# Kernel tuning notes

Measured on AMD Instinct MI355X. Metric: run time of the kernel, lower is better.

The kernel has to match this reference:

```python
import jax, jax.numpy as jnp
import numpy as np

N, E, T, F = 20000, 320000, 64, 16
HG, HT = 128, 256


def setup_inputs() -> dict:
    key = jax.random.key(0)
    ks = jax.random.split(key, 18)
    s = 0.05
    p = lambda k, shape: jax.random.normal(k, shape, jnp.float32) * s
    return {
        "x_seq": jax.random.normal(ks[0], (1, T, N, F), jnp.float32),
        "edge_index": jax.random.randint(ks[1], (2, E), 0, N, jnp.int32),
        # SAGEConv 1 (PyG default: mean aggregation; lin_l on aggregated neighbors w/ bias, lin_r on root w/o bias)
        "W1l": p(ks[2], (HG, F)), "b1l": p(ks[3], (HG,)), "W1r": p(ks[4], (HG, F)),
        # SAGEConv 2
        "W2l": p(ks[5], (HG, HG)), "b2l": p(ks[6], (HG,)), "W2r": p(ks[7], (HG, HG)),
        # GRU (torch gate order: r, z, n)
        "W_ih": p(ks[8], (3 * HT, HG)), "W_hh": p(ks[9], (3 * HT, HT)),
        "b_ih": p(ks[10], (3 * HT,)), "b_hh": p(ks[11], (3 * HT,)),
        # head: Linear(HT,64) -> ReLU -> Linear(64,1)
        "Wh1": p(ks[12], (64, HT)), "bh1": p(ks[13], (64,)),
        "Wh2": p(ks[14], (1, 64)), "bh2": p(ks[15], (1,)),
    }


def reference(x_seq, edge_index, W1l, b1l, W1r, W2l, b2l, W2r,
              W_ih, W_hh, b_ih, b_hh, Wh1, bh1, Wh2, bh2):
    n_nodes = x_seq.shape[2]
    src, dst = edge_index[0], edge_index[1]
    # in-degree for mean aggregation (0 -> output 0, matching scatter-mean)
    deg = jax.ops.segment_sum(jnp.ones(src.shape[0], x_seq.dtype), dst,
                              num_segments=n_nodes)
    inv_deg = jnp.where(deg > 0, 1.0 / deg, 0.0)[:, None]  # [N,1]

    def sage(x, Wl, bl, Wr):
        # mean over incoming neighbor messages, then linear + root linear
        agg = jax.ops.segment_sum(x[src], dst, num_segments=n_nodes) * inv_deg
        return agg @ Wl.T + bl + x @ Wr.T

    def graph_step(carry, x_t):  # x_t: [N, F]
        h = jax.nn.relu(sage(x_t, W1l, b1l, W1r))
        h = jax.nn.relu(sage(h, W2l, b2l, W2r))
        return carry, h.mean(axis=0)  # [HG]

    _, Hg = jax.lax.scan(graph_step, 0, x_seq[0])  # [T, HG]

    hidden_t = W_hh.shape[1]

    def gru_step(h, x_t):
        gi = x_t @ W_ih.T + b_ih
        gh = h @ W_hh.T + b_hh
        i_r, i_z, i_n = jnp.split(gi, 3)
        h_r, h_z, h_n = jnp.split(gh, 3)
        r = jax.nn.sigmoid(i_r + h_r)
        z = jax.nn.sigmoid(i_z + h_z)
        n = jnp.tanh(i_n + r * h_n)
        h_new = (1.0 - z) * n + z * h
        return h_new, h_new

    h0 = jnp.zeros((hidden_t,), x_seq.dtype)
    h_last, _ = jax.lax.scan(gru_step, h0, Hg)  # [HT]

    y = jax.nn.relu(h_last @ Wh1.T + bh1) @ Wh2.T + bh2  # [1]
    return y
```

## Files before the change

kernel.cpp:

```cpp
#include <hip/hip_runtime.h>
#include <hip/hip_bf16.h>

#define N_NODES 20000
#define N_EDGES 320000
#define T_STEPS 64
#define F_IN    16
#define HGd     128
#define HTd     256
#define INVN    (1.0f/20000.0f)
#define NTILES   625
#define S1T      79
#define NG64     313
#define QSCALE   64.0f
#define INVQ     (1.0f/64.0f)
#define QX       32.0f
#define INVQX    (1.0f/32.0f)
#define S_Q8     ((size_t)(N_NODES + 1) * HGd)

typedef __attribute__((ext_vector_type(8))) short short8;
typedef __attribute__((ext_vector_type(4))) float f32x4;
typedef __attribute__((ext_vector_type(2))) float f32x2;
typedef __attribute__((ext_vector_type(2))) _Float16 half2t;

static __device__ __forceinline__ ushort f2bf(float f) {
    __hip_bfloat16 b = __float2bfloat16(f);
    return *reinterpret_cast<ushort*>(&b);
}
static __device__ __forceinline__ half2t u2h(uint u) {
    half2t h; __builtin_memcpy(&h, &u, 4); return h;
}
static __device__ __forceinline__ uint packf16(float a, float b) {
    auto h = __builtin_amdgcn_cvt_pkrtz(a, b);
    uint u; __builtin_memcpy(&u, &h, 4); return u;
}

__global__ void k_zero(int* __restrict__ deg, float* __restrict__ HgP,
                       int* __restrict__ jobc, int* __restrict__ bins,
                       uint* __restrict__ h1q, int tch) {
    int i = blockIdx.x * blockDim.x + threadIdx.x;
    if (i < N_NODES) deg[i] = 0;
    if (i < T_STEPS * 8 * HGd) HgP[i] = 0.0f;
    if (i < 1024) jobc[i] = 0;
    if (i < 256) bins[i] = 0;
    if (i < tch * 32) {
        int sl = i >> 5, j = i & 31;
        h1q[sl * (S_Q8 / 4) + (size_t)N_NODES * (HGd / 4) + j] = 0u;
    }
}

__global__ void k_degree(const int* __restrict__ ei, int* __restrict__ deg) {
    int e = blockIdx.x * blockDim.x + threadIdx.x;
    if (e < N_EDGES) atomicAdd(&deg[ei[N_EDGES + e]], 1);
}

__global__ __launch_bounds__(1024) void k_scan(const int* __restrict__ deg,
        int* __restrict__ rp, int* __restrict__ cursor, float* __restrict__ invd) {
    __shared__ int sh[1024];
    __shared__ int carry_s;
    int tid = threadIdx.x;
    if (tid == 0) { carry_s = 0; rp[0] = 0; }
    __syncthreads();
    for (int base = 0; base < N_NODES; base += 1024) {
        int i = base + tid;
        int v = (i < N_NODES) ? deg[i] : 0;
        sh[tid] = v;
        __syncthreads();
        for (int off = 1; off < 1024; off <<= 1) {
            int t = (tid >= off) ? sh[tid - off] : 0;
            __syncthreads();
            sh[tid] += t;
            __syncthreads();
        }
        int inc = sh[tid] + carry_s;
        if (i < N_NODES) {
            rp[i + 1] = inc;
            cursor[i] = inc - v;
            invd[i] = (v > 0) ? (1.0f / (float)v) : 0.0f;
        }
        __syncthreads();
        if (tid == 1023) carry_s = inc;
        __syncthreads();
    }
}

__global__ void k_fill(const int* __restrict__ ei, int* __restrict__ cursor,
                       int* __restrict__ csr) {
    int e = blockIdx.x * blockDim.x + threadIdx.x;
    if (e < N_EDGES) {
        int d = ei[N_EDGES + e];
        int p = atomicAdd(&cursor[d], 1);
        csr[p] = ei[e];
    }
}

__global__ void k_hist(const int* __restrict__ deg, int* __restrict__ bins) {
    int i = blockIdx.x * blockDim.x + threadIdx.x;
    if (i < N_NODES) atomicAdd(&bins[min(deg[i], 255)], 1);
}

__global__ __launch_bounds__(256) void k_binscan(const int* __restrict__ bins,
        int* __restrict__ bincur, int* __restrict__ nodebefore,
        int* __restrict__ edgebefore, int* __restrict__ edgebp, int* __restrict__ rp2p) {
    __shared__ int sh[256], she[256], shp[256];
    int tid = threadIdx.x;
    int b = bins[tid];
    int dp = (tid + 7) & ~7;
    sh[tid] = b;
    she[tid] = b * tid;
    shp[tid] = b * dp;
    __syncthreads();
    for (int off = 1; off < 256; off <<= 1) {
        int v = (tid >= off) ? sh[tid - off] : 0;
        int ve = (tid >= off) ? she[tid - off] : 0;
        int vp = (tid >= off) ? shp[tid - off] : 0;
        __syncthreads();
        sh[tid] += v; she[tid] += ve; shp[tid] += vp;
        __syncthreads();
    }
    bincur[tid] = sh[tid] - b;
    nodebefore[tid] = sh[tid] - b;
    edgebefore[tid] = she[tid] - b * tid;
    edgebp[tid] = shp[tid] - b * dp;
    if (tid == 255) rp2p[N_NODES] = shp[255];
}

__global__ void k_perm(const int* __restrict__ deg, int* __restrict__ bincur,
                       const int* __restrict__ nodebefore, const int* __restrict__ edgebefore,
                       const int* __restrict__ edgebp, const float* __restrict__ invd,
                       int* __restrict__ perm, int* __restrict__ pos,
                       int* __restrict__ rp2, float* __restrict__ invd2,
                       int* __restrict__ degs2, int* __restrict__ rp2p) {
    int i = blockIdx.x * blockDim.x + threadIdx.x;
    if (i < N_NODES) {
        int d = min(deg[i], 255);
        int p = atomicAdd(&bincur[d], 1);
        int rank = p - nodebefore[d];
        perm[p] = i;
        pos[i] = p;
        rp2[p] = edgebefore[d] + rank * d;
        rp2p[p] = edgebp[d] + rank * ((d + 7) & ~7);
        invd2[p] = invd[i];
        degs2[p] = deg[i];
        if (i == 0) rp2[N_NODES] = N_EDGES;
    }
}

__global__ __launch_bounds__(512) void k_tb(const int* __restrict__ rp2, int* __restrict__ tb) {
    __shared__ int sh[512];
    int t = threadIdx.x;
    int md = 0;
    if (t < NG64 && t * 64 < N_NODES) {
        int last = min((t + 1) * 64, N_NODES) - 1;
        md = rp2[last + 1] - rp2[last];
    }
    sh[t] = 64 * md;
    __syncthreads();
    for (int off = 1; off < 512; off <<= 1) {
        int v = (t >= off) ? sh[t - off] : 0;
        __syncthreads();
        sh[t] += v;
        __syncthreads();
    }
    tb[t + 1] = sh[t];
    if (t == 0) tb[0] = 0;
}

__global__ void k_ecopy(const int* __restrict__ rp, const int* __restrict__ pos,
                        const int* __restrict__ rp2p, const int* __restrict__ tb,
                        const int* __restrict__ csr,
                        int* __restrict__ csr3, int* __restrict__ csr2p) {
    int e = blockIdx.x * blockDim.x + threadIdx.x;
    if (e < N_EDGES) {
        int lo = 0, hi = N_NODES - 1;
#pragma unroll
        for (int it = 0; it < 15; ++it) {
            int mid = (lo + hi + 1) >> 1;
            if (rp[mid] <= e) lo = mid; else hi = mid - 1;
        }
        int i = lo;
        int j = e - rp[i];
        int p = pos[i];
        int v = csr[e];
        csr3[tb[p >> 6] + j * 64 + (p & 63)] = v;
        csr2p[rp2p[p] + j] = v;
    }
}

__global__ void k_pad(const int* __restrict__ rp, const int* __restrict__ pos,
                      const int* __restrict__ rp2p, int* __restrict__ csr2p) {
    int i = blockIdx.x * blockDim.x + threadIdx.x;
    if (i < N_NODES) {
        int d = rp[i + 1] - rp[i];
        int dp = (d + 7) & ~7;
        int o = rp2p[pos[i]];
        for (int k = d; k < dp; ++k) csr2p[o + k] = N_NODES;
    }
}

__global__ void k_qx(const float* __restrict__ xs, int* __restrict__ x8, int n4) {
    int i = blockIdx.x * blockDim.x + threadIdx.x;
    if (i < n4) {
        float4 v = reinterpret_cast<const float4*>(xs)[i];
        int q8 = __builtin_amdgcn_cvt_pk_fp8_f32(v.x * QX, v.y * QX, 0, false);
        q8 = __builtin_amdgcn_cvt_pk_fp8_f32(v.z * QX, v.w * QX, q8, true);
        x8[i] = q8;
    }
}

__global__ void k_prepw(const float* __restrict__ W1l, const float* __restrict__ W1r,
                        const float* __restrict__ W2l, const float* __restrict__ W2r,
                        const float* __restrict__ W_ih, const float* __restrict__ W_hh,
                        ushort* __restrict__ W1T2, ushort* __restrict__ WT2,
                        float* __restrict__ WihT, uint* __restrict__ W_hhq) {
    int i = blockIdx.x * blockDim.x + threadIdx.x;
    const int n1 = 128 * 32, n2 = 128 * 256, n3 = 128 * 768, n4 = 128 * 768;
    if (i < n1) {
        int o = i >> 5, k = i & 31;
        float v = (k < 16) ? W1l[o * 16 + k] : W1r[o * 16 + (k - 16)];
        W1T2[i] = f2bf(v);
    } else if (i < n1 + n2) {
        int j = i - n1; int o = j >> 8, k = j & 255;
        float v = (k < 128) ? W2l[o * 128 + k] : W2r[o * 128 + (k - 128)];
        WT2[j] = f2bf(v);
    } else if (i < n1 + n2 + n3) {
        int j = i - n1 - n2; int k = j / 768, g = j % 768;
        WihT[j] = W_ih[g * 128 + k];
    } else if (i < n1 + n2 + n3 + n4) {
        int j = i - n1 - n2 - n3; int dw = j / 768, row = j % 768;
        float a = W_hh[(size_t)row * HTd + 2 * dw];
        float b = W_hh[(size_t)row * HTd + 2 * dw + 1];
        W_hhq[j] = packf16(a, b);
    }
}

__global__ __launch_bounds__(256) void k_sage1(
        const char* __restrict__ x8_, const int* __restrict__ tb,
        const int* __restrict__ csr3, const int* __restrict__ degs2,
        const float* __restrict__ invd2,
        const ushort* __restrict__ W1T2, const float* __restrict__ b1l,
        const int* __restrict__ perm, uchar1* __restrict__ h1q_,
        int* __restrict__ jobc, int C) {
    __shared__ ushort u[256 * 40];
    __shared__ int pnode[256];
    __shared__ int job_s;
    int tid = threadIdx.x;
    int l = tid & 63, w = tid >> 6;
    int lane15 = l & 15, g4 = l >> 4;
    const int xcd = blockIdx.x & 7;
    const int cmin = (C < 8) ? C : 8;
    const int ci = xcd % cmin;
    const int reps = (C >= 8) ? (C >> 3) : 1;
    int* ctr = jobc + ci;
    const int njobs = reps * S1T;

    short8 bfr1[2];
    float bb1[2];
#pragma unroll
    for (int ct = 0; ct < 2; ++ct) {
        int o16 = w * 32 + ct * 16 + lane15;
        bfr1[ct] = *reinterpret_cast<const short8*>(W1T2 + o16 * 32 + g4 * 8);
        bb1[ct] = b1l[o16];
    }

    for (;;) {
        if (tid == 0) job_s = atomicAdd(ctr, 1);
        __syncthreads();
        int job = job_s;
        if (job >= njobs) break;
        int rep = job / S1T;
        int tile = job - rep * S1T;
        int tl = ci + (rep << 3);
        const char* xq = x8_ + (size_t)tl * N_NODES * F_IN;
        char* h1q = (char*)h1q_ + (size_t)tl * S_Q8;
        int p = tile * 256 + tid;
        int node = (p < N_NODES) ? perm[p] : -1;
        pnode[tid] = node;

        float acc[16], rootv[16];
#pragma unroll
        for (int k = 0; k < 16; ++k) { acc[k] = 0.0f; rootv[k] = 0.0f; }
        if (node >= 0) {
            int d = degs2[p];
            const int base = tb[p >> 6] + (p & 63);
            for (int j = 0; j < d; ++j) {
                int idx = csr3[base + j * 64];
                uint4 row = *reinterpret_cast<const uint4*>(xq + (size_t)idx * F_IN);
#pragma unroll
                for (int c = 0; c < 4; ++c) {
                    uint vd = c == 0 ? row.x : c == 1 ? row.y : c == 2 ? row.z : row.w;
                    f32x2 lo = __builtin_amdgcn_cvt_pk_f32_fp8((int)vd, false);
                    f32x2 hi = __builtin_amdgcn_cvt_pk_f32_fp8((int)vd, true);
                    acc[4 * c + 0] += lo.x; acc[4 * c + 1] += lo.y;
                    acc[4 * c + 2] += hi.x; acc[4 * c + 3] += hi.y;
                }
            }
            float id = invd2[p] * INVQX;
#pragma unroll
            for (int k = 0; k < 16; ++k) acc[k] *= id;
            uint4 rv = *reinterpret_cast<const uint4*>(xq + (size_t)node * F_IN);
#pragma unroll
            for (int c = 0; c < 4; ++c) {
                uint vd = c == 0 ? rv.x : c == 1 ? rv.y : c == 2 ? rv.z : rv.w;
                f32x2 lo = __builtin_amdgcn_cvt_pk_f32_fp8((int)vd, false);
                f32x2 hi = __builtin_amdgcn_cvt_pk_f32_fp8((int)vd, true);
                rootv[4 * c + 0] = lo.x * INVQX; rootv[4 * c + 1] = lo.y * INVQX;
                rootv[4 * c + 2] = hi.x * INVQX; rootv[4 * c + 3] = hi.y * INVQX;
            }
        }
        {
            uint dw[16];
#pragma unroll
            for (int i = 0; i < 8; ++i)
                dw[i] = (uint)f2bf(acc[2 * i]) | ((uint)f2bf(acc[2 * i + 1]) << 16);
#pragma unroll
            for (int i = 0; i < 8; ++i)
                dw[8 + i] = (uint)f2bf(rootv[2 * i]) | ((uint)f2bf(rootv[2 * i + 1]) << 16);
            ushort* ur = u + tid * 40;
#pragma unroll
            for (int c = 0; c < 4; ++c)
                *reinterpret_cast<uint4*>(ur + c * 8) =
                    make_uint4(dw[4 * c], dw[4 * c + 1], dw[4 * c + 2], dw[4 * c + 3]);
        }
        __syncthreads();

#pragma unroll 4
        for (int rt = 0; rt < 16; ++rt) {
            int row = rt * 16 + lane15;
            short8 af = *reinterpret_cast<const short8*>(u + row * 40 + g4 * 8);
            f32x4 a0 = __builtin_amdgcn_mfma_f32_16x16x32_bf16(af, bfr1[0], (f32x4)(0.0f), 0, 0, 0);
            f32x4 a1 = __builtin_amdgcn_mfma_f32_16x16x32_bf16(af, bfr1[1], (f32x4)(0.0f), 0, 0, 0);
#pragma unroll
            for (int j = 0; j < 4; ++j) {
                int nl = rt * 16 + g4 * 4 + j;
                int nd = pnode[nl];
                if (nd >= 0) {
                    float v0 = fmaxf(a0[j] + bb1[0], 0.0f) * QSCALE;
                    float v1 = fmaxf(a1[j] + bb1[1], 0.0f) * QSCALE;
                    int q0 = __builtin_amdgcn_cvt_pk_fp8_f32(v0, v0, 0, false);
                    int q1 = __builtin_amdgcn_cvt_pk_fp8_f32(v1, v1, 0, false);
                    h1q[(size_t)nd * HGd + w * 32 + lane15] = (char)q0;
                    h1q[(size_t)nd * HGd + w * 32 + 16 + lane15] = (char)q1;
                }
            }
        }
    }
}

__global__ __launch_bounds__(256) void k_sage2(
        const uchar1* __restrict__ h1q_,
        const int* __restrict__ rp2p, const int* __restrict__ csr2p,
        const float* __restrict__ invd2,
        const ushort* __restrict__ WT2, const float* __restrict__ b2l,
        const int* __restrict__ perm, float* __restrict__ HgP,
        int* __restrict__ jobc, int t0, int C) {
    __shared__ uint4 usm4[32 * 512 / 16];
    __shared__ int pnode[32];
    __shared__ int job_s;
    char* ub = (char*)usm4;
    int tid = threadIdx.x;
    int l = tid & 63, w = tid >> 6;
    int lane15 = l & 15, g4 = l >> 4;
    const int xcd = blockIdx.x & 7;
    const int cmin = (C < 8) ? C : 8;
    const int ci = xcd % cmin;
    const int reps = (C >= 8) ? (C >> 3) : 1;
    int* ctr = jobc + ci;
    const int njobs = reps * NTILES;

    short8 bfr[2][8];
    float bb[2];
#pragma unroll
    for (int ct = 0; ct < 2; ++ct) {
        int n = w * 32 + ct * 16 + lane15;
        const ushort* bp = WT2 + n * 256 + g4 * 8;
#pragma unroll
        for (int ks = 0; ks < 8; ++ks)
            bfr[ct][ks] = *reinterpret_cast<const short8*>(bp + ks * 32);
        bb[ct] = b2l[n];
    }

    for (;;) {
        if (tid == 0) job_s = atomicAdd(ctr, 1);
        __syncthreads();
        int job = job_s;
        if (job >= njobs) break;
        int rep = job / NTILES;
        int tile = job - rep * NTILES;
        int tl = ci + ((reps - 1 - rep) << 3);
        int t = t0 + tl;
        const char* h1q = (const char*)h1q_ + (size_t)tl * S_Q8;
        int nbase = tile * 32;
        if (tid < 32) pnode[tid] = perm[nbase + tid];
        __syncthreads();

        {
            int nl = tid >> 3, seg = tid & 7;
            uint4 v = *reinterpret_cast<const uint4*>(h1q + (size_t)pnode[nl] * HGd + seg * 16);
            uint bw[8];
#pragma unroll
            for (int d = 0; d < 4; ++d) {
                uint vd = d == 0 ? v.x : d == 1 ? v.y : d == 2 ? v.z : v.w;
                f32x2 plo = __builtin_amdgcn_cvt_pk_f32_fp8((int)vd, false);
                f32x2 phi = __builtin_amdgcn_cvt_pk_f32_fp8((int)vd, true);
                bw[2 * d]     = (uint)f2bf(plo.x * INVQ) | ((uint)f2bf(plo.y * INVQ) << 16);
                bw[2 * d + 1] = (uint)f2bf(phi.x * INVQ) | ((uint)f2bf(phi.y * INVQ) << 16);
            }
            int base = nl * 512 + 256 + seg * 32;
            int swz = (nl & 7) << 4;
            *reinterpret_cast<uint4*>(ub + (base ^ swz)) =
                make_uint4(bw[0], bw[1], bw[2], bw[3]);
            *reinterpret_cast<uint4*>(ub + ((base + 16) ^ swz)) =
                make_uint4(bw[4], bw[5], bw[6], bw[7]);
        }

#pragma unroll
        for (int g = 0; g < 2; ++g) {
            int nl = w * 8 + g * 4 + g4;
            int sl = rp2p[nbase + nl];
            int dp = rp2p[nbase + nl + 1] - sl;
            const int* cp = csr2p + sl;
            float af[8] = {0, 0, 0, 0, 0, 0, 0, 0};
            if (dp > 0) {
                int idx[8];
#pragma unroll
                for (int uu = 0; uu < 8; ++uu) idx[uu] = cp[uu];
                for (int j = 0; j < dp; j += 8) {
                    uint2 vv[8];
#pragma unroll
                    for (int uu = 0; uu < 8; ++uu)
                        vv[uu] = *reinterpret_cast<const uint2*>(h1q + (size_t)idx[uu] * HGd + lane15 * 8);
                    cp += 8;
#pragma unroll
                    for (int uu = 0; uu < 8; ++uu) idx[uu] = cp[uu];
#pragma unroll
                    for (int uu = 0; uu < 8; ++uu) {
                        f32x2 p0 = __builtin_amdgcn_cvt_pk_f32_fp8((int)vv[uu].x, false);
                        f32x2 p1 = __builtin_amdgcn_cvt_pk_f32_fp8((int)vv[uu].x, true);
                        f32x2 p2 = __builtin_amdgcn_cvt_pk_f32_fp8((int)vv[uu].y, false);
                        f32x2 p3 = __builtin_amdgcn_cvt_pk_f32_fp8((int)vv[uu].y, true);
                        af[0] += p0.x; af[1] += p0.y; af[2] += p1.x; af[3] += p1.y;
                        af[4] += p2.x; af[5] += p2.y; af[6] += p3.x; af[7] += p3.y;
                    }
                }
            }
            float id = invd2[nbase + nl] * INVQ;
            uint4 pk;
            pk.x = (uint)f2bf(af[0] * id) | ((uint)f2bf(af[1] * id) << 16);
            pk.y = (uint)f2bf(af[2] * id) | ((uint)f2bf(af[3] * id) << 16);
            pk.z = (uint)f2bf(af[4] * id) | ((uint)f2bf(af[5] * id) << 16);
            pk.w = (uint)f2bf(af[6] * id) | ((uint)f2bf(af[7] * id) << 16);
            *reinterpret_cast<uint4*>(ub + ((nl * 512 + lane15 * 16) ^ ((nl & 7) << 4))) = pk;
        }
        __syncthreads();

        f32x4 acc[2][2];
#pragma unroll
        for (int rt = 0; rt < 2; ++rt)
#pragma unroll
            for (int ct = 0; ct < 2; ++ct) acc[rt][ct] = (f32x4)(0.0f);
#pragma unroll
        for (int ks = 0; ks < 8; ++ks) {
#pragma unroll
            for (int rt = 0; rt < 2; ++rt) {
                int row = rt * 16 + lane15;
                int byt = (row * 512 + (ks * 32 + g4 * 8) * 2) ^ ((row & 7) << 4);
                short8 af = *reinterpret_cast<const short8*>(ub + byt);
                acc[rt][0] = __builtin_amdgcn_mfma_f32_16x16x32_bf16(af, bfr[0][ks], acc[rt][0], 0, 0, 0);
                acc[rt][1] = __builtin_amdgcn_mfma_f32_16x16x32_bf16(af, bfr[1][ks], acc[rt][1], 0, 0, 0);
            }
        }
#pragma unroll
        for (int ct = 0; ct < 2; ++ct) {
            float sum = 0.f;
#pragma unroll
            for (int rt = 0; rt < 2; ++rt)
#pragma unroll
                for (int j = 0; j < 4; ++j)
                    sum += fmaxf(acc[rt][ct][j] + bb[ct], 0.f);
            sum += __shfl_xor(sum, 16);
            sum += __shfl_xor(sum, 32);
            if (g4 == 0) {
                int n = w * 32 + ct * 16 + lane15;
                atomicAdd(&HgP[(t * 8 + (tile & 7)) * HGd + n], sum);
            }
        }
    }
}

__global__ __launch_bounds__(768) void k_gi(const float* __restrict__ HgP,
        const float* __restrict__ WihT, const float* __restrict__ b_ih,
        float* __restrict__ gi_all) {
    __shared__ float x[HGd];
    int t = blockIdx.x, g = threadIdx.x;
    if (g < HGd) {
        float s = 0.f;
#pragma unroll
        for (int p = 0; p < 8; ++p) s += HgP[(t * 8 + p) * HGd + g];
        x[g] = s * INVN;
    }
    __syncthreads();
    float a = b_ih[g];
    for (int k = 0; k < HGd; ++k) a += WihT[k * 768 + g] * x[k];
    gi_all[t * 768 + g] = a;
}

__global__ __launch_bounds__(768, 3) void k_gru1b(const float* __restrict__ gi_all,
        const uint* __restrict__ W_hhq, const float* __restrict__ b_hh,
        const float* __restrict__ Wh1, const float* __restrict__ bh1,
        const float* __restrict__ Wh2, const float* __restrict__ bh2,
        float* __restrict__ out) {
    int tid = threadIdx.x;
    uint wv[128];
#pragma unroll
    for (int i = 0; i < 128; ++i) wv[i] = W_hhq[i * 768 + tid];
    float bh = b_hh[tid];

    __shared__ float hs[HTd];
    __shared__ uint h2s[HTd / 2];
    __shared__ float gh[3 * HTd];
    if (tid < HTd) hs[tid] = 0.0f;
    if (tid < HTd / 2) h2s[tid] = 0u;
    __syncthreads();

    for (int t = 0; t < T_STEPS; ++t) {
        float s = bh;
#pragma unroll
        for (int i = 0; i < 128; i += 4) {
            uint4 hh = *reinterpret_cast<const uint4*>(&h2s[i]);
            s = __builtin_amdgcn_fdot2(u2h(wv[i + 0]), u2h(hh.x), s, false);
            s = __builtin_amdgcn_fdot2(u2h(wv[i + 1]), u2h(hh.y), s, false);
            s = __builtin_amdgcn_fdot2(u2h(wv[i + 2]), u2h(hh.z), s, false);
            s = __builtin_amdgcn_fdot2(u2h(wv[i + 3]), u2h(hh.w), s, false);
        }
        gh[tid] = s;
        __syncthreads();
        if (tid < HTd) {
            float gir = gi_all[t * 768 + tid];
            float giz = gi_all[t * 768 + HTd + tid];
            float gin = gi_all[t * 768 + 2 * HTd + tid];
            float r = 1.0f / (1.0f + expf(-(gir + gh[tid])));
            float z = 1.0f / (1.0f + expf(-(giz + gh[HTd + tid])));
            float n = tanhf(gin + r * gh[2 * HTd + tid]);
            hs[tid] = (1.0f - z) * n + z * hs[tid];
        }
        __syncthreads();
        if (tid < HTd / 2)
            h2s[tid] = packf16(hs[2 * tid], hs[2 * tid + 1]);
        __syncthreads();
    }

    __shared__ float act[64];
    if (tid < 64) {
        float a = bh1[tid];
        const float* wr = Wh1 + tid * HTd;
        for (int k = 0; k < HTd; k += 4) {
            float4 wv4 = *reinterpret_cast<const float4*>(wr + k);
            a += wv4.x * hs[k] + wv4.y * hs[k + 1] + wv4.z * hs[k + 2] + wv4.w * hs[k + 3];
        }
        act[tid] = fmaxf(a, 0.0f);
    }
    __syncthreads();
    if (tid == 0) {
        float y = bh2[0];
        for (int j = 0; j < 64; ++j) y += Wh2[j] * act[j];
        out[0] = y;
    }
}

extern "C" void kernel_launch(void* const* d_in, const int* in_sizes, int n_in,
                              void* d_out, int out_size, void* d_ws, size_t ws_size,
                              hipStream_t stream) {
    const float* x_seq = (const float*)d_in[0];
    const int*   ei    = (const int*)d_in[1];
    const float* W1l   = (const float*)d_in[2];
    const float* b1l   = (const float*)d_in[3];
    const float* W1r   = (const float*)d_in[4];
    const float* W2l   = (const float*)d_in[5];
    const float* b2l   = (const float*)d_in[6];
    const float* W2r   = (const float*)d_in[7];
    const float* W_ih  = (const float*)d_in[8];
    const float* W_hh  = (const float*)d_in[9];
    const float* b_ih  = (const float*)d_in[10];
    const float* b_hh  = (const float*)d_in[11];
    const float* Wh1   = (const float*)d_in[12];
    const float* bh1   = (const float*)d_in[13];
    const float* Wh2   = (const float*)d_in[14];
    const float* bh2   = (const float*)d_in[15];
    float* out = (float*)d_out;

    char* ws = (char*)d_ws;
    size_t off = 0;
    auto take = [&](size_t nbytes) -> void* {
        void* p = (void*)(ws + off);
        off += (nbytes + 255) & ~(size_t)255;
        return p;
    };
    int*    deg    = (int*)take(N_NODES * 4);
    int*    rp     = (int*)take((N_NODES + 1) * 4);
    int*    cursor = (int*)take(N_NODES * 4);
    int*    csr    = (int*)take(N_EDGES * 4);
    float*  invd   = (float*)take(N_NODES * 4);
    int*    perm   = (int*)take(N_NODES * 4);
    int*    pos    = (int*)take(N_NODES * 4);
    int*    rp2    = (int*)take((N_NODES + 2) * 4);
    int*    rp2p   = (int*)take((N_NODES + 2) * 4);
    int*    csr2p  = (int*)take(480300 * 4);
    float*  invd2  = (float*)take(N_NODES * 4);
    int*    degs2  = (int*)take(N_NODES * 4);
    int*    tb     = (int*)take(520 * 4);
    int*    csr3   = (int*)take(360000 * 4);
    int*    bins   = (int*)take(256 * 4);
    int*    bincur = (int*)take(256 * 4);
    int*    nodeb  = (int*)take(256 * 4);
    int*    edgeb  = (int*)take(256 * 4);
    int*    edgebp = (int*)take(256 * 4);
    ushort* W1T2   = (ushort*)take(128 * 32 * 2);
    ushort* WT2    = (ushort*)take(128 * 256 * 2);
    float*  WihT   = (float*)take(128 * 768 * 4);
    uint*   W_hhq  = (uint*)take(128 * 768 * 4);
    float*  HgP    = (float*)take(T_STEPS * 8 * HGd * 4);
    float*  gi_all = (float*)take(T_STEPS * 768 * 4);
    int*    jobc   = (int*)take(1024 * 4);

    const size_t slice_q = (S_Q8 + 255) & ~(size_t)255;
    const size_t slice_x = ((size_t)N_NODES * F_IN + 255) & ~(size_t)255;
    int T_CH = 64;
    while (T_CH > 1 && off + (size_t)T_CH * (slice_q + slice_x) > ws_size)
        T_CH >>= 1;
    uchar1* h1q = (uchar1*)take((size_t)T_CH * slice_q);
    char*   x8  = (char*)take((size_t)T_CH * slice_x);

    k_zero<<<256, 256, 0, stream>>>(deg, HgP, jobc, bins, (uint*)h1q, T_CH);
    k_degree<<<(N_EDGES + 255) / 256, 256, 0, stream>>>(ei, deg);
    k_scan<<<1, 1024, 0, stream>>>(deg, rp, cursor, invd);
    k_fill<<<(N_EDGES + 255) / 256, 256, 0, stream>>>(ei, cursor, csr);
    k_hist<<<(N_NODES + 255) / 256, 256, 0, stream>>>(deg, bins);
    k_binscan<<<1, 256, 0, stream>>>(bins, bincur, nodeb, edgeb, edgebp, rp2p);
    k_perm<<<(N_NODES + 255) / 256, 256, 0, stream>>>(deg, bincur, nodeb, edgeb, edgebp,
                                                      invd, perm, pos, rp2, invd2, degs2, rp2p);
    k_tb<<<1, 512, 0, stream>>>(rp2, tb);
    k_ecopy<<<(N_EDGES + 255) / 256, 256, 0, stream>>>(rp, pos, rp2p, tb, csr, csr3, csr2p);
    k_pad<<<(N_NODES + 255) / 256, 256, 0, stream>>>(rp, pos, rp2p, csr2p);
    {
        int total = 128 * 32 + 128 * 256 + 128 * 768 + 128 * 768;
        k_prepw<<<(total + 255) / 256, 256, 0, stream>>>(W1l, W1r, W2l, W2r, W_ih, W_hh,
                                                         W1T2, WT2, WihT, W_hhq);
    }
    int chunk = 0;
    for (int t0 = 0; t0 < T_STEPS; t0 += T_CH, ++chunk) {
        int C = T_CH;
        int n4 = C * N_NODES * F_IN / 4;
        k_qx<<<(n4 + 255) / 256, 256, 0, stream>>>(
            x_seq + (size_t)t0 * N_NODES * F_IN, (int*)x8, n4);
        k_sage1<<<2048, 256, 0, stream>>>(x8, tb, csr3, degs2, invd2, W1T2, b1l, perm,
                                          h1q, jobc + chunk * 32, C);
        k_sage2<<<2048, 256, 0, stream>>>(h1q, rp2p, csr2p, invd2, WT2, b2l, perm, HgP,
                                          jobc + chunk * 32 + 16, t0, C);
    }
    k_gi<<<T_STEPS, 768, 0, stream>>>(HgP, WihT, b_ih, gi_all);
    k_gru1b<<<1, 768, 0, stream>>>(gi_all, W_hhq, b_hh, Wh1, bh1, Wh2, bh2, out);
}
```

Before: 1.021 ms.

## Double SAGE2 tile to 64 nodes and unroll SAGE1 gather by two

The second SAGE kernel now processes 64-node tiles instead of 32, so each job runs four MFMA row tiles against the register-resident weight fragments. This halves the number of job fetches and atomic adds to the pooled output, and bounds checks handle the ragged last tile. The first SAGE gather loop is unrolled by two so two neighbor loads are in flight at once. The larger tile doubles LDS use and adds accumulator registers, which may lower occupancy.

```diff
diff --git a/kernel.cpp b/kernel.cpp
--- a/kernel.cpp
+++ b/kernel.cpp
@@ -8,7 +8,7 @@
 #define HGd     128
 #define HTd     256
 #define INVN    (1.0f/20000.0f)
-#define NTILES   625
+#define NT64     313
 #define S1T      79
 #define NG64     313
 #define QSCALE   64.0f
@@ -282,7 +282,25 @@
         if (node >= 0) {
             int d = degs2[p];
             const int base = tb[p >> 6] + (p & 63);
-            for (int j = 0; j < d; ++j) {
+            int j = 0;
+            for (; j + 2 <= d; j += 2) {
+                int i0 = csr3[base + j * 64];
+                int i1 = csr3[base + (j + 1) * 64];
+                uint4 r0 = *reinterpret_cast<const uint4*>(xq + (size_t)i0 * F_IN);
+                uint4 r1 = *reinterpret_cast<const uint4*>(xq + (size_t)i1 * F_IN);
+#pragma unroll
+                for (int c = 0; c < 4; ++c) {
+                    uint v0 = c == 0 ? r0.x : c == 1 ? r0.y : c == 2 ? r0.z : r0.w;
+                    uint v1 = c == 0 ? r1.x : c == 1 ? r1.y : c == 2 ? r1.z : r1.w;
+                    f32x2 lo0 = __builtin_amdgcn_cvt_pk_f32_fp8((int)v0, false);
+                    f32x2 hi0 = __builtin_amdgcn_cvt_pk_f32_fp8((int)v0, true);
+                    f32x2 lo1 = __builtin_amdgcn_cvt_pk_f32_fp8((int)v1, false);
+                    f32x2 hi1 = __builtin_amdgcn_cvt_pk_f32_fp8((int)v1, true);
+                    acc[4 * c + 0] += lo0.x + lo1.x; acc[4 * c + 1] += lo0.y + lo1.y;
+                    acc[4 * c + 2] += hi0.x + hi1.x; acc[4 * c + 3] += hi0.y + hi1.y;
+                }
+            }
+            for (; j < d; ++j) {
                 int idx = csr3[base + j * 64];
                 uint4 row = *reinterpret_cast<const uint4*>(xq + (size_t)idx * F_IN);
 #pragma unroll
@@ -353,8 +371,8 @@
         const ushort* __restrict__ WT2, const float* __restrict__ b2l,
         const int* __restrict__ perm, float* __restrict__ HgP,
         int* __restrict__ jobc, int t0, int C) {
-    __shared__ uint4 usm4[32 * 512 / 16];
-    __shared__ int pnode[32];
+    __shared__ uint4 usm4[64 * 512 / 16];
+    __shared__ int pnode[64];
     __shared__ int job_s;
     char* ub = (char*)usm4;
     int tid = threadIdx.x;
@@ -365,7 +383,7 @@
     const int ci = xcd % cmin;
     const int reps = (C >= 8) ? (C >> 3) : 1;
     int* ctr = jobc + ci;
-    const int njobs = reps * NTILES;
+    const int njobs = reps * NT64;
 
     short8 bfr[2][8];
     float bb[2];
@@ -384,40 +402,48 @@
         __syncthreads();
         int job = job_s;
         if (job >= njobs) break;
-        int rep = job / NTILES;
-        int tile = job - rep * NTILES;
+        int rep = job / NT64;
+        int tile = job - rep * NT64;
         int tl = ci + ((reps - 1 - rep) << 3);
         int t = t0 + tl;
         const char* h1q = (const char*)h1q_ + (size_t)tl * S_Q8;
-        int nbase = tile * 32;
-        if (tid < 32) pnode[tid] = perm[nbase + tid];
+        int nbase = tile * 64;
+        if (tid < 64) {
+            int p = nbase + tid;
+            pnode[tid] = (p < N_NODES) ? perm[p] : N_NODES;
+        }
         __syncthreads();
 
         {
-            int nl = tid >> 3, seg = tid & 7;
-            uint4 v = *reinterpret_cast<const uint4*>(h1q + (size_t)pnode[nl] * HGd + seg * 16);
-            uint bw[8];
-#pragma unroll
-            for (int d = 0; d < 4; ++d) {
-                uint vd = d == 0 ? v.x : d == 1 ? v.y : d == 2 ? v.z : v.w;
-                f32x2 plo = __builtin_amdgcn_cvt_pk_f32_fp8((int)vd, false);
-                f32x2 phi = __builtin_amdgcn_cvt_pk_f32_fp8((int)vd, true);
-                bw[2 * d]     = (uint)f2bf(plo.x * INVQ) | ((uint)f2bf(plo.y * INVQ) << 16);
-                bw[2 * d + 1] = (uint)f2bf(phi.x * INVQ) | ((uint)f2bf(phi.y * INVQ) << 16);
-            }
-            int base = nl * 512 + 256 + seg * 32;
-            int swz = (nl & 7) << 4;
-            *reinterpret_cast<uint4*>(ub + (base ^ swz)) =
-                make_uint4(bw[0], bw[1], bw[2], bw[3]);
-            *reinterpret_cast<uint4*>(ub + ((base + 16) ^ swz)) =
-                make_uint4(bw[4], bw[5], bw[6], bw[7]);
-        }
-
-#pragma unroll
-        for (int g = 0; g < 2; ++g) {
-            int nl = w * 8 + g * 4 + g4;
-            int sl = rp2p[nbase + nl];
-            int dp = rp2p[nbase + nl + 1] - sl;
+            int nl = tid >> 2, sg2 = tid & 3;
+#pragma unroll
+            for (int h = 0; h < 2; ++h) {
+                int seg = sg2 * 2 + h;
+                uint4 v = *reinterpret_cast<const uint4*>(h1q + (size_t)pnode[nl] * HGd + seg * 16);
+                uint bw[8];
+#pragma unroll
+                for (int d = 0; d < 4; ++d) {
+                    uint vd = d == 0 ? v.x : d == 1 ? v.y : d == 2 ? v.z : v.w;
+                    f32x2 plo = __builtin_amdgcn_cvt_pk_f32_fp8((int)vd, false);
+                    f32x2 phi = __builtin_amdgcn_cvt_pk_f32_fp8((int)vd, true);
+                    bw[2 * d]     = (uint)f2bf(plo.x * INVQ) | ((uint)f2bf(plo.y * INVQ) << 16);
+                    bw[2 * d + 1] = (uint)f2bf(phi.x * INVQ) | ((uint)f2bf(phi.y * INVQ) << 16);
+                }
+                int base = nl * 512 + 256 + seg * 32;
+                int swz = (nl & 7) << 4;
+                *reinterpret_cast<uint4*>(ub + (base ^ swz)) =
+                    make_uint4(bw[0], bw[1], bw[2], bw[3]);
+                *reinterpret_cast<uint4*>(ub + ((base + 16) ^ swz)) =
+                    make_uint4(bw[4], bw[5], bw[6], bw[7]);
+            }
+        }
+
+#pragma unroll
+        for (int g = 0; g < 4; ++g) {
+            int nl = w * 16 + g * 4 + g4;
+            int p2 = nbase + nl;
+            int sl = 0, dp = 0;
+            if (p2 < N_NODES) { sl = rp2p[p2]; dp = rp2p[p2 + 1] - sl; }
             const int* cp = csr2p + sl;
             float af[8] = {0, 0, 0, 0, 0, 0, 0, 0};
             if (dp > 0) {
@@ -436,14 +462,14 @@
                     for (int uu = 0; uu < 8; ++uu) {
                         f32x2 p0 = __builtin_amdgcn_cvt_pk_f32_fp8((int)vv[uu].x, false);
                         f32x2 p1 = __builtin_amdgcn_cvt_pk_f32_fp8((int)vv[uu].x, true);
-                        f32x2 p2 = __builtin_amdgcn_cvt_pk_f32_fp8((int)vv[uu].y, false);
+                        f32x2 p2v = __builtin_amdgcn_cvt_pk_f32_fp8((int)vv[uu].y, false);
                         f32x2 p3 = __builtin_amdgcn_cvt_pk_f32_fp8((int)vv[uu].y, true);
                         af[0] += p0.x; af[1] += p0.y; af[2] += p1.x; af[3] += p1.y;
-                        af[4] += p2.x; af[5] += p2.y; af[6] += p3.x; af[7] += p3.y;
+                        af[4] += p2v.x; af[5] += p2v.y; af[6] += p3.x; af[7] += p3.y;
                     }
                 }
             }
-            float id = invd2[nbase + nl] * INVQ;
+            float id = (p2 < N_NODES) ? invd2[p2] * INVQ : 0.0f;
             uint4 pk;
             pk.x = (uint)f2bf(af[0] * id) | ((uint)f2bf(af[1] * id) << 16);
             pk.y = (uint)f2bf(af[2] * id) | ((uint)f2bf(af[3] * id) << 16);
@@ -453,15 +479,15 @@
         }
         __syncthreads();
 
-        f32x4 acc[2][2];
-#pragma unroll
-        for (int rt = 0; rt < 2; ++rt)
+        f32x4 acc[4][2];
+#pragma unroll
+        for (int rt = 0; rt < 4; ++rt)
 #pragma unroll
             for (int ct = 0; ct < 2; ++ct) acc[rt][ct] = (f32x4)(0.0f);
 #pragma unroll
         for (int ks = 0; ks < 8; ++ks) {
 #pragma unroll
-            for (int rt = 0; rt < 2; ++rt) {
+            for (int rt = 0; rt < 4; ++rt) {
                 int row = rt * 16 + lane15;
                 int byt = (row * 512 + (ks * 32 + g4 * 8) * 2) ^ ((row & 7) << 4);
                 short8 af = *reinterpret_cast<const short8*>(ub + byt);
@@ -473,10 +499,13 @@
         for (int ct = 0; ct < 2; ++ct) {
             float sum = 0.f;
 #pragma unroll
-            for (int rt = 0; rt < 2; ++rt)
-#pragma unroll
-                for (int j = 0; j < 4; ++j)
-                    sum += fmaxf(acc[rt][ct][j] + bb[ct], 0.f);
+            for (int rt = 0; rt < 4; ++rt)
+#pragma unroll
+                for (int j = 0; j < 4; ++j) {
+                    int rowi = rt * 16 + g4 * 4 + j;
+                    float v = fmaxf(acc[rt][ct][j] + bb[ct], 0.f);
+                    sum += (nbase + rowi < N_NODES) ? v : 0.f;
+                }
             sum += __shfl_xor(sum, 16);
             sum += __shfl_xor(sum, 32);
             if (g4 == 0) {
```

Measured after the change: 1.298 ms. 1.27x slower.
